# Kernel optimization log

Hardware: AMD Instinct MI355X
Metric: run time of the kernel (lower is better)

## Reference

```python
import jax, jax.numpy as jnp
import numpy as np
from jax.ops import segment_sum

N_NODES = 100000


def setup_inputs() -> dict:
    key = jax.random.key(0)
    k1, k2, k3, k4, k5 = jax.random.split(key, 5)
    E = 3200000
    x = jax.random.normal(k1, (N_NODES, 8), dtype=jnp.float32)
    edge_index = jax.random.randint(k2, (2, E), 0, N_NODES, dtype=jnp.int64)
    edge_attr = jax.random.uniform(k3, (E,), dtype=jnp.float32)
    W = jax.random.normal(k4, (8, 64), dtype=jnp.float32) * (1.0 / np.sqrt(8.0))
    b = jax.random.normal(k5, (64,), dtype=jnp.float32) * 0.01
    return {"x": x, "edge_index": edge_index, "edge_attr": edge_attr, "W": W, "b": b}


def reference(x, edge_index, edge_attr, W, b):
    # GCNConv(8, 64) with symmetric normalization and self-loops (PyG defaults).
    N = x.shape[0]
    # Add self-loops with weight 1.0
    loops = jnp.arange(N, dtype=edge_index.dtype)
    row = jnp.concatenate([edge_index[0], loops])            # source nodes [E+N]
    col = jnp.concatenate([edge_index[1], loops])            # target nodes [E+N]
    ew = jnp.concatenate([edge_attr, jnp.ones((N,), dtype=edge_attr.dtype)])
    # Symmetric degree normalization: deg computed on target index
    deg = segment_sum(ew, col, num_segments=N)               # [N]
    dis = jnp.where(deg > 0, jax.lax.rsqrt(jnp.where(deg > 0, deg, 1.0)), 0.0)
    norm = dis[row] * ew * dis[col]                          # [E+N]
    # Linear transform first (in=8 -> out=64), then gather/scale/scatter-add
    xt = x @ W                                               # [N, 64]
    msgs = xt[row] * norm[:, None]                           # [E+N, 64]
    out = segment_sum(msgs, col, num_segments=N) + b         # [N, 64]
    return out
```

## Files before the change

### kernel.cpp

```cpp
#include <hip/hip_runtime.h>


#define NBMAX 1024
#define PSH   7
#define BINSZ 128
#define TILE  6144
#define EPT   6
#define CAP   6144

static inline size_t ws_align(size_t x) { return (x + 255) & ~(size_t)255; }

__global__ void init_k(const unsigned* w, unsigned* orw, int E) {
    int t = threadIdx.x;
    __shared__ unsigned s;
    if (t == 0) s = 0u;
    __syncthreads();
    unsigned v = 0;
    int lim = (E < 2048) ? E : 2048;
    for (int i = t; i < lim; i += 256)
        v |= w[2 * i + 1];
    atomicOr(&s, v);
    __syncthreads();
    if (t == 0) *orw = s;
}

__global__ __launch_bounds__(1024)
void hist_k(const void* ei, const unsigned* orw, unsigned* tcnt,
            int E, int NB, int ntiles) {
    __shared__ unsigned lh[NBMAX];
    const bool is64 = (*orw == 0u);
    const int* e32 = (const int*)ei;
    const long long* e64 = (const long long*)ei;
    const int t = threadIdx.x;
    for (int tile = blockIdx.x; tile < ntiles; tile += gridDim.x) {
        int base = tile * TILE;
        int tc = E - base; if (tc > TILE) tc = TILE;
        for (int i = t; i < NB; i += 1024) lh[i] = 0u;
        __syncthreads();
        for (int e = base + t; e < base + tc; e += 1024) {
            int c = is64 ? (int)e64[E + e] : e32[E + e];
            atomicAdd(&lh[c >> PSH], 1u);
        }
        __syncthreads();
        for (int i = t; i < NB; i += 1024)
            tcnt[(size_t)tile * NB + i] = lh[i];
        __syncthreads();
    }
}

__global__ void scan2_k(unsigned* tcnt, unsigned* cnt, int NB, int ntiles) {
    int b = blockIdx.x, lane = threadIdx.x;
    unsigned run = 0;
    for (int base = 0; base < ntiles; base += 64) {
        int i = base + lane;
        unsigned v = (i < ntiles) ? tcnt[(size_t)i * NB + b] : 0u;
        unsigned s = v;
        #pragma unroll
        for (int d = 1; d < 64; d <<= 1) {
            unsigned u = __shfl_up(s, d);
            if (lane >= d) s += u;
        }
        if (i < ntiles) tcnt[(size_t)i * NB + b] = run + s - v;
        run += __shfl(s, 63);
    }
    if (lane == 0) cnt[b] = run;
}

__global__ void scan_k(const unsigned* cnt, unsigned* offs, int NB) {
    __shared__ unsigned wsum[16];
    int t = threadIdx.x, lane = t & 63, wv = t >> 6;
    unsigned v0 = (t < NB) ? cnt[t] : 0u;
    unsigned s = v0;
    #pragma unroll
    for (int d = 1; d < 64; d <<= 1) {
        unsigned u = __shfl_up(s, d);
        if (lane >= d) s += u;
    }
    if (lane == 63) wsum[wv] = s;
    __syncthreads();
    if (t < 16) {
        unsigned w = wsum[t];
        #pragma unroll
        for (int d = 1; d < 16; d <<= 1) {
            unsigned u = __shfl_up(w, d, 16);
            if (t >= d) w += u;
        }
        wsum[t] = w;
    }
    __syncthreads();
    unsigned excl = s - v0 + (wv ? wsum[wv - 1] : 0u);
    if (t < NB) offs[t] = excl;
    if (t == NB - 1) offs[NB] = excl + v0;
}

__global__ __launch_bounds__(1024)
void scat_k(const void* ei, const float* ea, const unsigned* orw,
            const unsigned* offs, const unsigned* tcnt,
            unsigned long long* pay, int E, int NB, int ntiles, int cpx) {
    __shared__ unsigned long long lp[TILE];
    __shared__ unsigned short lbin[TILE];
    __shared__ unsigned lh[NBMAX];
    __shared__ unsigned lo[NBMAX];
    __shared__ unsigned tb[NBMAX];
    __shared__ unsigned wsum[16];
    const bool is64 = (*orw == 0u);
    const int* e32 = (const int*)ei;
    const long long* e64 = (const long long*)ei;
    const int t = threadIdx.x, lane = t & 63, wv = t >> 6;
    const int sgrid = cpx * 8;

    for (int ii = blockIdx.x; ii < sgrid; ii += gridDim.x) {
        int tile = (ii & 7) * cpx + (ii >> 3);
        if (tile >= ntiles) continue;
        int base = tile * TILE;
        int tc = E - base; if (tc > TILE) tc = TILE;

        for (int i = t; i < NB; i += 1024) lh[i] = 0u;
        __syncthreads();

        int bn[EPT]; unsigned rk[EPT]; unsigned long long pv[EPT];
        #pragma unroll
        for (int i = 0; i < EPT; ++i) {
            int e = base + i * 1024 + t;
            bn[i] = -1;
            if (e < base + tc) {
                int c, r;
                if (is64) { c = (int)e64[E + e]; r = (int)e64[e]; }
                else      { c = e32[E + e];      r = e32[e]; }
                float w = ea[e];
                bn[i] = c >> PSH;
                pv[i] = ((unsigned long long)__float_as_uint(w) << 32)
                        | ((unsigned)r << 8) | (unsigned)(c & (BINSZ - 1));
                rk[i] = atomicAdd(&lh[bn[i]], 1u);
            }
        }
        __syncthreads();

        unsigned v0 = (t < NB) ? lh[t] : 0u;
        unsigned s = v0;
        #pragma unroll
        for (int d = 1; d < 64; d <<= 1) {
            unsigned u = __shfl_up(s, d);
            if (lane >= d) s += u;
        }
        if (lane == 63) wsum[wv] = s;
        __syncthreads();
        if (t < 16) {
            unsigned w = wsum[t];
            #pragma unroll
            for (int d = 1; d < 16; d <<= 1) {
                unsigned u = __shfl_up(w, d, 16);
                if (t >= d) w += u;
            }
            wsum[t] = w;
        }
        __syncthreads();
        unsigned excl = s - v0 + (wv ? wsum[wv - 1] : 0u);
        if (t < NB) {
            lo[t] = excl;
            tb[t] = offs[t] + tcnt[(size_t)tile * NB + t];
        }
        __syncthreads();

        #pragma unroll
        for (int i = 0; i < EPT; ++i)
            if (bn[i] >= 0) {
                unsigned pos = lo[bn[i]] + rk[i];
                lp[pos] = pv[i];
                lbin[pos] = (unsigned short)bn[i];
            }
        __syncthreads();

        for (int q = t; q < tc; q += 1024) {
            int a = lbin[q];
            pay[(size_t)tb[a] + (unsigned)q - lo[a]] = lp[q];
        }
        __syncthreads();
    }
}

__global__ __launch_bounds__(1024)
void nodestat_k(const unsigned long long* pay, const unsigned* offs,
                unsigned* noffs, float* dis, const float* x, float* y,
                int N, int E) {
    __shared__ unsigned cnt[BINSZ];
    __shared__ float dw[BINSZ];
    __shared__ float sdis[BINSZ];
    __shared__ unsigned wpart[2];
    int b = blockIdx.x, t = threadIdx.x, lane = t & 63, wv = t >> 6;
    if (t < BINSZ) { cnt[t] = 0u; dw[t] = 0.f; }
    if (b == 0 && t == 0) noffs[N] = (unsigned)E;
    __syncthreads();
    unsigned base = offs[b], len = offs[b + 1] - base;
    for (unsigned j = t; j < len; j += 1024) {
        unsigned long long p = pay[base + j];
        unsigned lc = (unsigned)p & 255u;
        atomicAdd(&cnt[lc], 1u);
        atomicAdd(&dw[lc], __uint_as_float((unsigned)(p >> 32)));
    }
    __syncthreads();
    unsigned v0 = (t < BINSZ) ? cnt[t] : 0u;
    unsigned s = v0;
    #pragma unroll
    for (int d = 1; d < 64; d <<= 1) {
        unsigned u = __shfl_up(s, d);
        if (lane >= d) s += u;
    }
    if (t < BINSZ && lane == 63) wpart[wv] = s;
    __syncthreads();
    if (t < BINSZ) {
        unsigned excl = s - v0 + (wv == 1 ? wpart[0] : 0u);
        int node = b * BINSZ + t;
        float dval = 0.f;
        if (node < N) {
            noffs[node] = base + excl;
            float d = 1.0f + dw[t];
            dval = (d > 0.f) ? rsqrtf(d) : 0.f;
            dis[node] = dval;
        }
        sdis[t] = dval;
    }
    __syncthreads();
    int gi = b * (BINSZ * 8) + t;
    if (gi < N * 8) y[gi] = sdis[t >> 3] * x[gi];
}

__global__ __launch_bounds__(1024)
void aggfuse_k(const unsigned long long* pay, const unsigned* offs,
               const unsigned* noffs, const float* dis, const float* y,
               const float* Wm, const float* bv, float* out, int N) {
    __shared__ unsigned long long lp[CAP];
    __shared__ float spill[BINSZ][8];
    __shared__ float sag[BINSZ][8];
    __shared__ unsigned loc[BINSZ];
    __shared__ unsigned cur[BINSZ];
    const float4* y4 = (const float4*)y;
    int b = blockIdx.x, t = threadIdx.x, lane = t & 63, wv = t >> 6;
    unsigned base = offs[b], len = offs[b + 1] - base;
    ((float*)spill)[t] = 0.f;
    if (t < BINSZ) {
        int node = b * BINSZ + t;
        unsigned l = (node < N) ? (noffs[node] - base) : len;
        loc[t] = l; cur[t] = l;
    }
    __syncthreads();
    for (unsigned j = t; j < len; j += 1024) {
        unsigned long long p = pay[base + j];
        unsigned lc = (unsigned)p & 255u;
        unsigned pos = atomicAdd(&cur[lc], 1u);
        if (pos < CAP) lp[pos] = p;
        else {
            unsigned r = ((unsigned)p >> 8) & 0xFFFFFFu;
            float ew = __uint_as_float((unsigned)(p >> 32));
            float4 u = y4[(size_t)r * 2], v = y4[(size_t)r * 2 + 1];
            atomicAdd(&spill[lc][0], ew * u.x); atomicAdd(&spill[lc][1], ew * u.y);
            atomicAdd(&spill[lc][2], ew * u.z); atomicAdd(&spill[lc][3], ew * u.w);
            atomicAdd(&spill[lc][4], ew * v.x); atomicAdd(&spill[lc][5], ew * v.y);
            atomicAdd(&spill[lc][6], ew * v.z); atomicAdd(&spill[lc][7], ew * v.w);
        }
    }
    __syncthreads();
    int quad = lane >> 4;
    int l4 = lane & 15;
    int slot = l4 >> 1, h = l4 & 1;
    for (int i = 0; i < 2; ++i) {
        int ln = wv + ((4 * i + quad) << 4);
        int node = b * BINSZ + ln;
        float a0 = 0.f, a1 = 0.f, a2 = 0.f, a3 = 0.f;
        if (node < N) {
            unsigned s = loc[ln] + slot;
            unsigned e = (ln < BINSZ - 1) ? loc[ln + 1] : len;
            e = e < CAP ? e : CAP;
            for (unsigned j = s; j < e; j += 8) {
                unsigned long long p = lp[j];
                unsigned r = ((unsigned)p >> 8) & 0xFFFFFFu;
                float ew = __uint_as_float((unsigned)(p >> 32));
                float4 v = y4[(size_t)r * 2 + h];
                a0 += ew * v.x; a1 += ew * v.y; a2 += ew * v.z; a3 += ew * v.w;
            }
        }
        #pragma unroll
        for (int m = 2; m <= 8; m <<= 1) {
            a0 += __shfl_xor(a0, m); a1 += __shfl_xor(a1, m);
            a2 += __shfl_xor(a2, m); a3 += __shfl_xor(a3, m);
        }
        if (slot == 0 && node < N) {
            float dc = dis[node];
            float4 vy = y4[(size_t)node * 2 + h];
            sag[ln][h * 4 + 0] = dc * (a0 + spill[ln][h * 4 + 0] + vy.x);
            sag[ln][h * 4 + 1] = dc * (a1 + spill[ln][h * 4 + 1] + vy.y);
            sag[ln][h * 4 + 2] = dc * (a2 + spill[ln][h * 4 + 2] + vy.z);
            sag[ln][h * 4 + 3] = dc * (a3 + spill[ln][h * 4 + 3] + vy.w);
        }
    }
    __syncthreads();
    float wr[8];
    #pragma unroll
    for (int k = 0; k < 8; ++k) wr[k] = Wm[k * 64 + lane];
    float bj = bv[lane];
    for (int i = 0; i < 8; ++i) {
        int ln = wv + (i << 4);
        int node = b * BINSZ + ln;
        if (node < N) {
            float o = bj;
            #pragma unroll
            for (int k = 0; k < 8; ++k) o += sag[ln][k] * wr[k];
            out[(size_t)node * 64 + lane] = o;
        }
    }
}

__global__ void fb_init_k(float* deg, float4* agg4, int N) {
    int i = blockIdx.x * blockDim.x + threadIdx.x, st = gridDim.x * blockDim.x;
    for (; i < N; i += st) {
        deg[i] = 1.0f;
        agg4[2 * i] = make_float4(0.f, 0.f, 0.f, 0.f);
        agg4[2 * i + 1] = make_float4(0.f, 0.f, 0.f, 0.f);
    }
}
__global__ void fb_deg_k(const void* ei, const float* ea, const unsigned* orw,
                         float* deg, int E) {
    const bool is64 = (*orw == 0u);
    const int* e32 = (const int*)ei;
    const long long* e64 = (const long long*)ei;
    int e = blockIdx.x * blockDim.x + threadIdx.x, st = gridDim.x * blockDim.x;
    for (; e < E; e += st) {
        int c = is64 ? (int)e64[E + e] : e32[E + e];
        atomicAdd(&deg[c], ea[e]);
    }
}
__global__ void fb_dis_k(float* deg, int N) {
    int i = blockIdx.x * blockDim.x + threadIdx.x, st = gridDim.x * blockDim.x;
    for (; i < N; i += st) {
        float d = deg[i];
        deg[i] = (d > 0.f) ? rsqrtf(d) : 0.f;
    }
}
__global__ void fb_edge_k(const void* ei, const float* ea, const unsigned* orw,
                          const float* dis, const float* x, float* agg, int E) {
    const bool is64 = (*orw == 0u);
    const int* e32 = (const int*)ei;
    const long long* e64 = (const long long*)ei;
    int e = blockIdx.x * blockDim.x + threadIdx.x, st = gridDim.x * blockDim.x;
    for (; e < E; e += st) {
        int r, c;
        if (is64) { r = (int)e64[e]; c = (int)e64[E + e]; }
        else      { r = e32[e];      c = e32[E + e]; }
        float nrm = dis[r] * ea[e] * dis[c];
        const float4* xr = (const float4*)(x + (size_t)r * 8);
        float4 a = xr[0], bb = xr[1];
        float* ag = agg + (size_t)c * 8;
        atomicAdd(ag + 0, nrm * a.x);  atomicAdd(ag + 1, nrm * a.y);
        atomicAdd(ag + 2, nrm * a.z);  atomicAdd(ag + 3, nrm * a.w);
        atomicAdd(ag + 4, nrm * bb.x); atomicAdd(ag + 5, nrm * bb.y);
        atomicAdd(ag + 6, nrm * bb.z); atomicAdd(ag + 7, nrm * bb.w);
    }
}
__global__ void fb_out_k(const float* x, const float* Wm, const float* bv,
                         const float* dis, const float* agg, float* out, int N) {
    int lane = threadIdx.x & 63;
    int wid = blockIdx.x * (blockDim.x >> 6) + (threadIdx.x >> 6);
    int nw = gridDim.x * (blockDim.x >> 6);
    float wr[8];
    #pragma unroll
    for (int k = 0; k < 8; ++k) wr[k] = Wm[k * 64 + lane];
    float bj = bv[lane];
    for (int i = wid; i < N; i += nw) {
        float d = dis[i];
        float ink = 0.f;
        if (lane < 8) ink = agg[(size_t)i * 8 + lane] + d * d * x[(size_t)i * 8 + lane];
        float acc = bj;
        #pragma unroll
        for (int k = 0; k < 8; ++k) acc += __shfl(ink, k) * wr[k];
        out[(size_t)i * 64 + lane] = acc;
    }
}

extern "C" void kernel_launch(void* const* d_in, const int* in_sizes, int n_in,
                              void* d_out, int out_size, void* d_ws, size_t ws_size,
                              hipStream_t stream) {
    const float* x  = (const float*)d_in[0];
    const void*  ei = d_in[1];
    const float* ea = (const float*)d_in[2];
    const float* Wm = (const float*)d_in[3];
    const float* bv = (const float*)d_in[4];
    float* out = (float*)d_out;

    const int N = in_sizes[0] / 8;
    const int E = in_sizes[2];
    const int NB = (N + BINSZ - 1) / BINSZ;
    const int ntiles = (E + TILE - 1) / TILE;
    const int cpx = (ntiles + 7) / 8;

    char* ws = (char*)d_ws;
    size_t o = 0;
    unsigned* orw   = (unsigned*)(ws + o); o += 256;
    unsigned* cnt   = (unsigned*)(ws + o); o += ws_align(NBMAX * 4);
    unsigned* offs  = (unsigned*)(ws + o); o += ws_align((NBMAX + 1) * 4);
    float* dis      = (float*)(ws + o);    o += ws_align((size_t)N * 4);
    unsigned* noffs = (unsigned*)(ws + o); o += ws_align((size_t)(N + 1) * 4);
    float* y        = (float*)(ws + o);    o += ws_align((size_t)N * 8 * 4);
    unsigned* tcnt  = (unsigned*)(ws + o); o += ws_align((size_t)ntiles * NB * 4);
    unsigned long long* pay = (unsigned long long*)(ws + o);
    o += ws_align((size_t)E * 8);

    if (NB <= NBMAX && E >= 2048 && o <= ws_size) {
        int hgrid = ntiles < 2048 ? ntiles : 2048;
        int sgrid = cpx * 8 < 2048 ? cpx * 8 : 2048;
        init_k<<<1, 256, 0, stream>>>((const unsigned*)ei, orw, E);
        hist_k<<<hgrid, 1024, 0, stream>>>(ei, orw, tcnt, E, NB, ntiles);
        scan2_k<<<NB, 64, 0, stream>>>(tcnt, cnt, NB, ntiles);
        scan_k<<<1, 1024, 0, stream>>>(cnt, offs, NB);
        scat_k<<<sgrid, 1024, 0, stream>>>(ei, ea, orw, offs, tcnt, pay, E, NB,
                                           ntiles, cpx);
        nodestat_k<<<NB, 1024, 0, stream>>>(pay, offs, noffs, dis, x, y, N, E);
        aggfuse_k<<<NB, 1024, 0, stream>>>(pay, offs, noffs, dis, y, Wm, bv, out, N);
    } else {
        float* agg = (float*)(ws + 256 + ws_align((size_t)N * 4));
        init_k<<<1, 256, 0, stream>>>((const unsigned*)ei, orw, E);
        fb_init_k<<<(N + 255) / 256, 256, 0, stream>>>(dis, (float4*)agg, N);
        fb_deg_k<<<2048, 256, 0, stream>>>(ei, ea, orw, dis, E);
        fb_dis_k<<<(N + 255) / 256, 256, 0, stream>>>(dis, N);
        fb_edge_k<<<2048, 256, 0, stream>>>(ei, ea, orw, dis, x, agg, E);
        fb_out_k<<<2048, 256, 0, stream>>>(x, Wm, bv, dis, agg, out, N);
    }
}
```

Measured before the change: 108.2 us.

## Drop init kernel, inline dtype detection, replace sorted aggregation with shared atomics

Removes the single-block init kernel and has hist_k and scat_k each detect the int32/int64 index layout from the first words of the input. Drops the per-node counting and prefix scan in the degree kernel and the local counting-sort plus spill path in the aggregation kernel. Each edge now accumulates its weighted y row directly into a padded shared-memory accumulator with float atomics. This saves one launch and the in-block sort and scan, at the cost of heavy shared-atomic contention (8 atomics per edge) and a redundant detection read in every block.

```diff
diff --git a/kernel.cpp b/kernel.cpp
--- a/kernel.cpp
+++ b/kernel.cpp
@@ -6,29 +6,25 @@
 #define BINSZ 128
 #define TILE  6144
 #define EPT   6
-#define CAP   6144
 
 static inline size_t ws_align(size_t x) { return (x + 255) & ~(size_t)255; }
 
-__global__ void init_k(const unsigned* w, unsigned* orw, int E) {
-    int t = threadIdx.x;
-    __shared__ unsigned s;
-    if (t == 0) s = 0u;
-    __syncthreads();
+__device__ __forceinline__ bool detect64(const unsigned* w, int E) {
+    __shared__ unsigned det;
+    if (threadIdx.x == 0) det = 0u;
+    __syncthreads();
+    int lim = E < 1024 ? E : 1024;
     unsigned v = 0;
-    int lim = (E < 2048) ? E : 2048;
-    for (int i = t; i < lim; i += 256)
-        v |= w[2 * i + 1];
-    atomicOr(&s, v);
-    __syncthreads();
-    if (t == 0) *orw = s;
+    for (int i = threadIdx.x; i < lim; i += blockDim.x) v |= w[2 * i + 1];
+    if (v) atomicOr(&det, 1u);
+    __syncthreads();
+    return det == 0u;
 }
 
 __global__ __launch_bounds__(1024)
-void hist_k(const void* ei, const unsigned* orw, unsigned* tcnt,
-            int E, int NB, int ntiles) {
+void hist_k(const void* ei, unsigned* tcnt, int E, int NB, int ntiles) {
     __shared__ unsigned lh[NBMAX];
-    const bool is64 = (*orw == 0u);
+    const bool is64 = detect64((const unsigned*)ei, E);
     const int* e32 = (const int*)ei;
     const long long* e64 = (const long long*)ei;
     const int t = threadIdx.x;
@@ -94,16 +90,16 @@
 }
 
 __global__ __launch_bounds__(1024)
-void scat_k(const void* ei, const float* ea, const unsigned* orw,
-            const unsigned* offs, const unsigned* tcnt,
-            unsigned long long* pay, int E, int NB, int ntiles, int cpx) {
+void scat_k(const void* ei, const float* ea, const unsigned* offs,
+            const unsigned* tcnt, unsigned long long* pay,
+            int E, int NB, int ntiles, int cpx) {
     __shared__ unsigned long long lp[TILE];
     __shared__ unsigned short lbin[TILE];
     __shared__ unsigned lh[NBMAX];
     __shared__ unsigned lo[NBMAX];
     __shared__ unsigned tb[NBMAX];
     __shared__ unsigned wsum[16];
-    const bool is64 = (*orw == 0u);
+    const bool is64 = detect64((const unsigned*)ei, E);
     const int* e32 = (const int*)ei;
     const long long* e64 = (const long long*)ei;
     const int t = threadIdx.x, lane = t & 63, wv = t >> 6;
@@ -180,40 +176,23 @@
 }
 
 __global__ __launch_bounds__(1024)
-void nodestat_k(const unsigned long long* pay, const unsigned* offs,
-                unsigned* noffs, float* dis, const float* x, float* y,
-                int N, int E) {
-    __shared__ unsigned cnt[BINSZ];
+void deg_k(const unsigned long long* pay, const unsigned* offs,
+           float* dis, const float* x, float* y, int N) {
     __shared__ float dw[BINSZ];
     __shared__ float sdis[BINSZ];
-    __shared__ unsigned wpart[2];
-    int b = blockIdx.x, t = threadIdx.x, lane = t & 63, wv = t >> 6;
-    if (t < BINSZ) { cnt[t] = 0u; dw[t] = 0.f; }
-    if (b == 0 && t == 0) noffs[N] = (unsigned)E;
+    int b = blockIdx.x, t = threadIdx.x;
+    if (t < BINSZ) dw[t] = 0.f;
     __syncthreads();
     unsigned base = offs[b], len = offs[b + 1] - base;
     for (unsigned j = t; j < len; j += 1024) {
         unsigned long long p = pay[base + j];
-        unsigned lc = (unsigned)p & 255u;
-        atomicAdd(&cnt[lc], 1u);
-        atomicAdd(&dw[lc], __uint_as_float((unsigned)(p >> 32)));
-    }
-    __syncthreads();
-    unsigned v0 = (t < BINSZ) ? cnt[t] : 0u;
-    unsigned s = v0;
-    #pragma unroll
-    for (int d = 1; d < 64; d <<= 1) {
-        unsigned u = __shfl_up(s, d);
-        if (lane >= d) s += u;
-    }
-    if (t < BINSZ && lane == 63) wpart[wv] = s;
+        atomicAdd(&dw[(unsigned)p & 255u], __uint_as_float((unsigned)(p >> 32)));
+    }
     __syncthreads();
     if (t < BINSZ) {
-        unsigned excl = s - v0 + (wv == 1 ? wpart[0] : 0u);
         int node = b * BINSZ + t;
         float dval = 0.f;
         if (node < N) {
-            noffs[node] = base + excl;
             float d = 1.0f + dw[t];
             dval = (d > 0.f) ? rsqrtf(d) : 0.f;
             dis[node] = dval;
@@ -226,72 +205,26 @@
 }
 
 __global__ __launch_bounds__(1024)
-void aggfuse_k(const unsigned long long* pay, const unsigned* offs,
-               const unsigned* noffs, const float* dis, const float* y,
-               const float* Wm, const float* bv, float* out, int N) {
-    __shared__ unsigned long long lp[CAP];
-    __shared__ float spill[BINSZ][8];
-    __shared__ float sag[BINSZ][8];
-    __shared__ unsigned loc[BINSZ];
-    __shared__ unsigned cur[BINSZ];
+void agg_k(const unsigned long long* pay, const unsigned* offs,
+           const float* dis, const float* y, const float* Wm, const float* bv,
+           float* out, int N) {
+    __shared__ float sag[BINSZ][9];
     const float4* y4 = (const float4*)y;
     int b = blockIdx.x, t = threadIdx.x, lane = t & 63, wv = t >> 6;
+    for (int i = t; i < BINSZ * 9; i += 1024) ((float*)sag)[i] = 0.f;
+    __syncthreads();
     unsigned base = offs[b], len = offs[b + 1] - base;
-    ((float*)spill)[t] = 0.f;
-    if (t < BINSZ) {
-        int node = b * BINSZ + t;
-        unsigned l = (node < N) ? (noffs[node] - base) : len;
-        loc[t] = l; cur[t] = l;
-    }
-    __syncthreads();
     for (unsigned j = t; j < len; j += 1024) {
         unsigned long long p = pay[base + j];
-        unsigned lc = (unsigned)p & 255u;
-        unsigned pos = atomicAdd(&cur[lc], 1u);
-        if (pos < CAP) lp[pos] = p;
-        else {
-            unsigned r = ((unsigned)p >> 8) & 0xFFFFFFu;
-            float ew = __uint_as_float((unsigned)(p >> 32));
-            float4 u = y4[(size_t)r * 2], v = y4[(size_t)r * 2 + 1];
-            atomicAdd(&spill[lc][0], ew * u.x); atomicAdd(&spill[lc][1], ew * u.y);
-            atomicAdd(&spill[lc][2], ew * u.z); atomicAdd(&spill[lc][3], ew * u.w);
-            atomicAdd(&spill[lc][4], ew * v.x); atomicAdd(&spill[lc][5], ew * v.y);
-            atomicAdd(&spill[lc][6], ew * v.z); atomicAdd(&spill[lc][7], ew * v.w);
-        }
-    }
-    __syncthreads();
-    int quad = lane >> 4;
-    int l4 = lane & 15;
-    int slot = l4 >> 1, h = l4 & 1;
-    for (int i = 0; i < 2; ++i) {
-        int ln = wv + ((4 * i + quad) << 4);
-        int node = b * BINSZ + ln;
-        float a0 = 0.f, a1 = 0.f, a2 = 0.f, a3 = 0.f;
-        if (node < N) {
-            unsigned s = loc[ln] + slot;
-            unsigned e = (ln < BINSZ - 1) ? loc[ln + 1] : len;
-            e = e < CAP ? e : CAP;
-            for (unsigned j = s; j < e; j += 8) {
-                unsigned long long p = lp[j];
-                unsigned r = ((unsigned)p >> 8) & 0xFFFFFFu;
-                float ew = __uint_as_float((unsigned)(p >> 32));
-                float4 v = y4[(size_t)r * 2 + h];
-                a0 += ew * v.x; a1 += ew * v.y; a2 += ew * v.z; a3 += ew * v.w;
-            }
-        }
-        #pragma unroll
-        for (int m = 2; m <= 8; m <<= 1) {
-            a0 += __shfl_xor(a0, m); a1 += __shfl_xor(a1, m);
-            a2 += __shfl_xor(a2, m); a3 += __shfl_xor(a3, m);
-        }
-        if (slot == 0 && node < N) {
-            float dc = dis[node];
-            float4 vy = y4[(size_t)node * 2 + h];
-            sag[ln][h * 4 + 0] = dc * (a0 + spill[ln][h * 4 + 0] + vy.x);
-            sag[ln][h * 4 + 1] = dc * (a1 + spill[ln][h * 4 + 1] + vy.y);
-            sag[ln][h * 4 + 2] = dc * (a2 + spill[ln][h * 4 + 2] + vy.z);
-            sag[ln][h * 4 + 3] = dc * (a3 + spill[ln][h * 4 + 3] + vy.w);
-        }
+        unsigned lw = (unsigned)p;
+        int lc = lw & 255u;
+        unsigned r = (lw >> 8) & 0xFFFFFFu;
+        float ew = __uint_as_float((unsigned)(p >> 32));
+        float4 u = y4[(size_t)r * 2], v = y4[(size_t)r * 2 + 1];
+        atomicAdd(&sag[lc][0], ew * u.x); atomicAdd(&sag[lc][1], ew * u.y);
+        atomicAdd(&sag[lc][2], ew * u.z); atomicAdd(&sag[lc][3], ew * u.w);
+        atomicAdd(&sag[lc][4], ew * v.x); atomicAdd(&sag[lc][5], ew * v.y);
+        atomicAdd(&sag[lc][6], ew * v.z); atomicAdd(&sag[lc][7], ew * v.w);
     }
     __syncthreads();
     float wr[8];
@@ -302,20 +235,34 @@
         int ln = wv + (i << 4);
         int node = b * BINSZ + ln;
         if (node < N) {
+            float dc = dis[node];
             float o = bj;
             #pragma unroll
-            for (int k = 0; k < 8; ++k) o += sag[ln][k] * wr[k];
+            for (int k = 0; k < 8; ++k)
+                o += dc * (sag[ln][k] + y[(size_t)node * 8 + k]) * wr[k];
             out[(size_t)node * 64 + lane] = o;
         }
     }
 }
 
-__global__ void fb_init_k(float* deg, float4* agg4, int N) {
+__global__ void fb_init_k(const unsigned* w, unsigned* orw, float* deg,
+                          float4* agg4, int N, int E) {
     int i = blockIdx.x * blockDim.x + threadIdx.x, st = gridDim.x * blockDim.x;
     for (; i < N; i += st) {
         deg[i] = 1.0f;
         agg4[2 * i] = make_float4(0.f, 0.f, 0.f, 0.f);
         agg4[2 * i + 1] = make_float4(0.f, 0.f, 0.f, 0.f);
+    }
+    if (blockIdx.x == 0) {
+        __shared__ unsigned s;
+        if (threadIdx.x == 0) s = 0u;
+        __syncthreads();
+        unsigned v = 0;
+        int lim = (E < 2048) ? E : 2048;
+        for (int k = threadIdx.x; k < lim; k += blockDim.x) v |= w[2 * k + 1];
+        atomicOr(&s, v);
+        __syncthreads();
+        if (threadIdx.x == 0) *orw = s;
     }
 }
 __global__ void fb_deg_k(const void* ei, const float* ea, const unsigned* orw,
@@ -394,31 +341,29 @@
 
     char* ws = (char*)d_ws;
     size_t o = 0;
-    unsigned* orw   = (unsigned*)(ws + o); o += 256;
-    unsigned* cnt   = (unsigned*)(ws + o); o += ws_align(NBMAX * 4);
-    unsigned* offs  = (unsigned*)(ws + o); o += ws_align((NBMAX + 1) * 4);
-    float* dis      = (float*)(ws + o);    o += ws_align((size_t)N * 4);
-    unsigned* noffs = (unsigned*)(ws + o); o += ws_align((size_t)(N + 1) * 4);
-    float* y        = (float*)(ws + o);    o += ws_align((size_t)N * 8 * 4);
-    unsigned* tcnt  = (unsigned*)(ws + o); o += ws_align((size_t)ntiles * NB * 4);
+    unsigned* orw  = (unsigned*)(ws + o); o += 256;
+    unsigned* cnt  = (unsigned*)(ws + o); o += ws_align(NBMAX * 4);
+    unsigned* offs = (unsigned*)(ws + o); o += ws_align((NBMAX + 1) * 4);
+    float* dis     = (float*)(ws + o);    o += ws_align((size_t)N * 4);
+    float* y       = (float*)(ws + o);    o += ws_align((size_t)N * 8 * 4);
+    unsigned* tcnt = (unsigned*)(ws + o); o += ws_align((size_t)ntiles * NB * 4);
     unsigned long long* pay = (unsigned long long*)(ws + o);
     o += ws_align((size_t)E * 8);
 
     if (NB <= NBMAX && E >= 2048 && o <= ws_size) {
         int hgrid = ntiles < 2048 ? ntiles : 2048;
         int sgrid = cpx * 8 < 2048 ? cpx * 8 : 2048;
-        init_k<<<1, 256, 0, stream>>>((const unsigned*)ei, orw, E);
-        hist_k<<<hgrid, 1024, 0, stream>>>(ei, orw, tcnt, E, NB, ntiles);
+        hist_k<<<hgrid, 1024, 0, stream>>>(ei, tcnt, E, NB, ntiles);
         scan2_k<<<NB, 64, 0, stream>>>(tcnt, cnt, NB, ntiles);
         scan_k<<<1, 1024, 0, stream>>>(cnt, offs, NB);
-        scat_k<<<sgrid, 1024, 0, stream>>>(ei, ea, orw, offs, tcnt, pay, E, NB,
+        scat_k<<<sgrid, 1024, 0, stream>>>(ei, ea, offs, tcnt, pay, E, NB,
                                            ntiles, cpx);
-        nodestat_k<<<NB, 1024, 0, stream>>>(pay, offs, noffs, dis, x, y, N, E);
-        aggfuse_k<<<NB, 1024, 0, stream>>>(pay, offs, noffs, dis, y, Wm, bv, out, N);
+        deg_k<<<NB, 1024, 0, stream>>>(pay, offs, dis, x, y, N);
+        agg_k<<<NB, 1024, 0, stream>>>(pay, offs, dis, y, Wm, bv, out, N);
     } else {
         float* agg = (float*)(ws + 256 + ws_align((size_t)N * 4));
-        init_k<<<1, 256, 0, stream>>>((const unsigned*)ei, orw, E);
-        fb_init_k<<<(N + 255) / 256, 256, 0, stream>>>(dis, (float4*)agg, N);
+        fb_init_k<<<(N + 255) / 256, 256, 0, stream>>>((const unsigned*)ei, orw,
+                                                       dis, (float4*)agg, N, E);
         fb_deg_k<<<2048, 256, 0, stream>>>(ei, ea, orw, dis, E);
         fb_dis_k<<<(N + 255) / 256, 256, 0, stream>>>(dis, N);
         fb_edge_k<<<2048, 256, 0, stream>>>(ei, ea, orw, dis, x, agg, E);
```

Result: slower. 245.9 us (+127.3%).
